# Optimization experiments

Measured on AMD Instinct MI355X. Metric: run time of the kernel, lower is better.

Reference implementation:

```python
import jax, jax.numpy as jnp
import numpy as np
import math

HIDDEN = 1024
N_HEADS = 16
HEAD_DIM = HIDDEN // N_HEADS
N_BLOCKS = 16
BATCH = 2
SEQ = 4096


def setup_inputs() -> dict:
    key = jax.random.key(0)
    ks = jax.random.split(key, 8)
    attention_input = jax.random.normal(ks[0], (BATCH, SEQ, HIDDEN), dtype=jnp.float32)
    attention_mask = jnp.ones((BATCH, SEQ), dtype=jnp.float32)
    # permutation over the num_blocks*num_heads flattened (block, head) axis
    permutation = jax.random.permutation(ks[1], N_BLOCKS * N_HEADS)
    init = 0.02
    q_w = jax.random.normal(ks[2], (HIDDEN, N_HEADS, HEAD_DIM), dtype=jnp.float32) * init
    q_b = jax.random.normal(ks[3], (N_HEADS, HEAD_DIM), dtype=jnp.float32) * init
    k_w = jax.random.normal(ks[4], (HIDDEN, N_HEADS, HEAD_DIM), dtype=jnp.float32) * init
    k_b = jax.random.normal(ks[5], (N_HEADS, HEAD_DIM), dtype=jnp.float32) * init
    v_w = jax.random.normal(ks[6], (HIDDEN, N_HEADS, HEAD_DIM), dtype=jnp.float32) * init
    v_b = jax.random.normal(ks[7], (N_HEADS, HEAD_DIM), dtype=jnp.float32) * init
    return {"attention_input": attention_input, "attention_mask": attention_mask,
            "permutation": permutation, "q_w": q_w, "q_b": q_b,
            "k_w": k_w, "k_b": k_b, "v_w": v_w, "v_b": v_b}


def reference(attention_input, attention_mask, permutation, q_w, q_b, k_w, k_b, v_w, v_b):
    B = attention_mask.shape[0]
    S = attention_mask.shape[1]
    nb = N_BLOCKS
    nh, d = q_b.shape
    blk = S // nb
    # QKV projections: [B,S,H] x [H,N,D] -> [B,S,N,D]
    q = jnp.einsum('bsh,hnd->bsnd', attention_input, q_w) + q_b
    k = jnp.einsum('bsh,hnd->bsnd', attention_input, k_w) + k_b
    v = jnp.einsum('bsh,hnd->bsnd', attention_input, v_w) + v_b

    def blockify(x):  # [B,S,N,D] -> [B, nb, nh, blk, d]
        return x.reshape(B, nb, blk, nh, d).transpose(0, 1, 3, 2, 4)

    q = blockify(q)
    # flatten (block, head) axis and gather per permutation
    k = blockify(k).reshape(B, nb * nh, blk, d)[:, permutation].reshape(B, nb, nh, blk, d)
    v = blockify(v).reshape(B, nb * nh, blk, d)[:, permutation].reshape(B, nb, nh, blk, d)

    scale = 1.0 / math.sqrt(float(d))
    logits = jnp.einsum('bgnqd,bgnkd->bgnqk', q, k) * scale  # block-local scores
    attn = jax.nn.softmax(logits, axis=-1)  # dropout prob 0 / eval mode
    ctx = jnp.einsum('bgnqk,bgnkd->bgnqd', attn, v)
    # [B,nb,nh,blk,d] -> [B,nb,blk,nh,d] -> [B,S,nh,d]
    return ctx.transpose(0, 1, 3, 2, 4).reshape(B, S, nh, d)
```

## Files before the change

kernel.cpp:

```cpp
#include <hip/hip_runtime.h>
#include <hip/hip_bf16.h>
#include <stdint.h>

typedef __attribute__((ext_vector_type(4))) float f32x4;
typedef __attribute__((ext_vector_type(8))) short s16x8;

__device__ inline short f2bf(float f) {
  union { float f; uint32_t u; } v; v.f = f;
  uint32_t r = v.u + 0x7fffu + ((v.u >> 16) & 1u);
  return (short)(r >> 16);
}

__device__ inline void gload_lds16(const void* g, void* l) {
  __builtin_amdgcn_global_load_lds((const __attribute__((address_space(1))) void*)g,
                                   (__attribute__((address_space(3))) void*)l,
                                   16, 0, 0);
}

__global__ __launch_bounds__(256) void k_convert_x(const float* __restrict__ x,
                                                   short* __restrict__ xb) {
  int i = (blockIdx.x * 256 + threadIdx.x) * 8;
  const float4* p = (const float4*)(x + i);
  float4 a = p[0], b = p[1];
  s16x8 o;
  o[0] = f2bf(a.x); o[1] = f2bf(a.y); o[2] = f2bf(a.z); o[3] = f2bf(a.w);
  o[4] = f2bf(b.x); o[5] = f2bf(b.y); o[6] = f2bf(b.z); o[7] = f2bf(b.w);
  *(s16x8*)(xb + i) = o;
}

__global__ __launch_bounds__(256) void k_transpose_w(const float* __restrict__ qw,
                                                     const float* __restrict__ kw,
                                                     const float* __restrict__ vw,
                                                     short* __restrict__ wt) {
  __shared__ float tile[64][65];
  int a  = blockIdx.x >> 8;
  int t2 = blockIdx.x & 255;
  int k0 = (t2 >> 4) << 6;
  int n0 = (t2 & 15) << 6;
  const float* w = (a == 0) ? qw : (a == 1) ? kw : vw;
  int c = threadIdx.x & 63, rr = threadIdx.x >> 6;
#pragma unroll
  for (int i = 0; i < 16; ++i) {
    int r = i * 4 + rr;
    tile[r][c] = w[(k0 + r) * 1024 + n0 + c];
  }
  __syncthreads();
  short* o = wt + a * 1048576;
#pragma unroll
  for (int i = 0; i < 16; ++i) {
    int r = i * 4 + rr;
    o[(n0 + r) * 1024 + k0 + c] = f2bf(tile[c][r]);
  }
}

__global__ __launch_bounds__(256, 2) void k_gemm(const short* __restrict__ xb,
                                                 const short* __restrict__ wt,
                                                 const float* __restrict__ qbias,
                                                 const float* __restrict__ kbias,
                                                 const float* __restrict__ vbias,
                                                 short* __restrict__ Qo,
                                                 short* __restrict__ Ko,
                                                 short* __restrict__ Vo) {
  __shared__ short lds[36864];
  const int tid = threadIdx.x, lane = tid & 63, wv = tid >> 6;
  const int wm = wv >> 1, wn = wv & 1;
  const int mt = blockIdx.x, by = blockIdx.y;
  const int a = by >> 3;
  const short* asrc = xb + (size_t)(mt * 256) * 1024;
  const short* bsrc = wt + (size_t)a * 1048576 + (size_t)((by & 7) * 128) * 1024;

  int srcA[4], dstA[4], srcB[2], dstB[2];
#pragma unroll
  for (int i = 0; i < 4; ++i) {
    int L = i * 256 + tid, s = L & 31;
    int row = (L >> 5) * 8 + (s >> 2);
    int c = (s & 3) ^ ((s >> 3) & 3);
    srcA[i] = row * 1024 + c * 8;
    dstA[i] = L * 16;
  }
#pragma unroll
  for (int i = 0; i < 2; ++i) {
    int L = i * 256 + tid, s = L & 31;
    int row = (L >> 5) * 8 + (s >> 2);
    int c = (s & 3) ^ ((s >> 3) & 3);
    srcB[i] = row * 1024 + c * 8;
    dstB[i] = 16384 + L * 16;
  }

  int aoff[8], boff[4];
#pragma unroll
  for (int m = 0; m < 8; ++m) {
    int row = wm * 128 + m * 16 + (lane & 15);
    aoff[m] = ((row >> 3) * 32 + (row & 7) * 4 + ((lane >> 4) ^ ((row >> 1) & 3))) * 16;
  }
#pragma unroll
  for (int n = 0; n < 4; ++n) {
    int row = wn * 64 + n * 16 + (lane & 15);
    boff[n] = 16384 + ((row >> 3) * 32 + (row & 7) * 4 + ((lane >> 4) ^ ((row >> 1) & 3))) * 16;
  }

  f32x4 acc[8][4] = {};

  auto STAGE = [&](int t, int bb) {
    const short* at = asrc + t * 32;
    const short* bt = bsrc + t * 32;
    char* l = (char*)lds + bb;
#pragma unroll
    for (int i = 0; i < 4; ++i) gload_lds16(at + srcA[i], l + dstA[i]);
#pragma unroll
    for (int i = 0; i < 2; ++i) gload_lds16(bt + srcB[i], l + dstB[i]);
  };

  STAGE(0, 0);
  STAGE(1, 24576);
  int bcur = 0, bpre = 49152;

  for (int t = 0; t < 31; ++t) {
    asm volatile("s_waitcnt vmcnt(6)" ::: "memory");
    __builtin_amdgcn_s_barrier();
    asm volatile("" ::: "memory");
    if (t < 30) STAGE(t + 2, bpre);
    const char* bufc = (const char*)lds + bcur;
    s16x8 af[8], bf[4];
#pragma unroll
    for (int m = 0; m < 8; ++m) af[m] = *(const s16x8*)(bufc + aoff[m]);
#pragma unroll
    for (int n = 0; n < 4; ++n) bf[n] = *(const s16x8*)(bufc + boff[n]);
    __builtin_amdgcn_s_setprio(1);
#pragma unroll
    for (int m = 0; m < 8; ++m)
#pragma unroll
      for (int n = 0; n < 4; ++n)
        acc[m][n] = __builtin_amdgcn_mfma_f32_16x16x32_bf16(af[m], bf[n], acc[m][n], 0, 0, 0);
    __builtin_amdgcn_s_setprio(0);
    bcur += 24576; if (bcur == 73728) bcur = 0;
    bpre += 24576; if (bpre == 73728) bpre = 0;
  }
  asm volatile("s_waitcnt vmcnt(0)" ::: "memory");
  __builtin_amdgcn_s_barrier();
  asm volatile("" ::: "memory");
  {
    const char* bufc = (const char*)lds + bcur;
    s16x8 af[8], bf[4];
#pragma unroll
    for (int m = 0; m < 8; ++m) af[m] = *(const s16x8*)(bufc + aoff[m]);
#pragma unroll
    for (int n = 0; n < 4; ++n) bf[n] = *(const s16x8*)(bufc + boff[n]);
    __builtin_amdgcn_s_setprio(1);
#pragma unroll
    for (int m = 0; m < 8; ++m)
#pragma unroll
      for (int n = 0; n < 4; ++n)
        acc[m][n] = __builtin_amdgcn_mfma_f32_16x16x32_bf16(af[m], bf[n], acc[m][n], 0, 0, 0);
    __builtin_amdgcn_s_setprio(0);
  }

  const float* bias = (a == 0) ? qbias : (a == 1) ? kbias : vbias;
  short* outp = (a == 0) ? Qo : (a == 1) ? Ko : Vo;
  int nbase = (by & 7) * 128 + wn * 64;
  int mbase = mt * 256 + wm * 128;
#pragma unroll
  for (int n = 0; n < 4; ++n) {
    int nloc = nbase + n * 16 + (lane & 15);
    float bv = bias[nloc];
#pragma unroll
    for (int m = 0; m < 8; ++m)
#pragma unroll
      for (int r = 0; r < 4; ++r) {
        int mm = mbase + m * 16 + ((lane >> 4) << 2) + r;
        outp[(size_t)mm * 1024 + nloc] = f2bf(acc[m][n][r] + bv);
      }
  }
}

__global__ __launch_bounds__(512) void k_attn(const short* __restrict__ Qb,
                                              const short* __restrict__ Kb,
                                              const short* __restrict__ Vb,
                                              const int* __restrict__ perm,
                                              float* __restrict__ out) {
  __shared__ short Qs[256 * 64];
  __shared__ short Ks[256 * 64];
  __shared__ short Vs[64 * 256];
  __shared__ short Ps[8 * 1024];

  int tid = threadIdx.x;
  int lane = tid & 63, wv = tid >> 6;
  int bx = blockIdx.x;
  int b = bx >> 8, g = (bx >> 4) & 15, n = bx & 15;
  int p = perm[g * 16 + n];
  int pg = p >> 4, ph = p & 15;

  const short* qsrc = Qb + (size_t)(b * 4096 + g * 256) * 1024 + n * 64;
  const short* ksrc = Kb + (size_t)(b * 4096 + pg * 256) * 1024 + ph * 64;
  const short* vsrc = Vb + (size_t)(b * 4096 + pg * 256) * 1024 + ph * 64;

  s16x8 vreg[4];
#pragma unroll
  for (int i = 0; i < 4; ++i) {
    int c = i * 512 + tid;
    int t = c >> 3;
    int d0 = (c & 7) << 3;
    vreg[i] = *(const s16x8*)(vsrc + t * 1024 + d0);
  }
#pragma unroll
  for (int i = 0; i < 4; ++i) {
    int c = i * 512 + tid;
    int row = c >> 3;
    int colb = (c & 7) << 4;
    int sc = colb ^ ((row & 7) << 4);
    gload_lds16(qsrc + row * 1024 + (sc >> 1), (char*)Qs + c * 16);
    gload_lds16(ksrc + row * 1024 + (sc >> 1), (char*)Ks + c * 16);
  }
#pragma unroll
  for (int i = 0; i < 4; ++i) {
    int c = i * 512 + tid;
    int t = c >> 3;
    int d0 = (c & 7) << 3;
#pragma unroll
    for (int j = 0; j < 8; ++j) {
      int d = d0 + j;
      int sl = (d & 7) ^ ((d >> 3) & 7);
      int by = d * 512 + ((t * 2) ^ (sl << 4));
      *(short*)((char*)Vs + by) = vreg[i][j];
    }
  }
  __syncthreads();

  int qr0 = wv * 32;
  f32x4 accS[2][16] = {};
#pragma unroll
  for (int ks = 0; ks < 2; ++ks) {
    int cb = (ks << 6) + ((lane >> 4) << 4);
    s16x8 aq[2];
#pragma unroll
    for (int rf = 0; rf < 2; ++rf) {
      int row = qr0 + rf * 16 + (lane & 15);
      aq[rf] = *(const s16x8*)((const char*)Qs + row * 128 + (cb ^ ((row & 7) << 4)));
    }
#pragma unroll
    for (int cf = 0; cf < 16; ++cf) {
      int row = cf * 16 + (lane & 15);
      s16x8 bk = *(const s16x8*)((const char*)Ks + row * 128 + (cb ^ ((row & 7) << 4)));
      accS[0][cf] = __builtin_amdgcn_mfma_f32_16x16x32_bf16(aq[0], bk, accS[0][cf], 0, 0, 0);
      accS[1][cf] = __builtin_amdgcn_mfma_f32_16x16x32_bf16(aq[1], bk, accS[1][cf], 0, 0, 0);
    }
  }

  const float sc_log2e = 0.125f * 1.44269504088896f;
  float mx[2][4], inv[2][4];
#pragma unroll
  for (int rf = 0; rf < 2; ++rf)
#pragma unroll
    for (int r = 0; r < 4; ++r) {
      float m_ = accS[rf][0][r];
#pragma unroll
      for (int cf = 1; cf < 16; ++cf) m_ = fmaxf(m_, accS[rf][cf][r]);
#pragma unroll
      for (int msk = 1; msk < 16; msk <<= 1) m_ = fmaxf(m_, __shfl_xor(m_, msk));
      mx[rf][r] = m_;
    }
#pragma unroll
  for (int rf = 0; rf < 2; ++rf)
#pragma unroll
    for (int r = 0; r < 4; ++r) {
      float s_ = 0.f;
#pragma unroll
      for (int cf = 0; cf < 16; ++cf) {
        float e = exp2f((accS[rf][cf][r] - mx[rf][r]) * sc_log2e);
        accS[rf][cf][r] = e;
        s_ += e;
      }
#pragma unroll
      for (int msk = 1; msk < 16; msk <<= 1) s_ += __shfl_xor(s_, msk);
      inv[rf][r] = 1.0f / s_;
    }

  f32x4 accO[2][4] = {};
  short* pchunk = Ps + wv * 1024;
#pragma unroll
  for (int ks = 0; ks < 8; ++ks) {
#pragma unroll
    for (int rf = 0; rf < 2; ++rf)
#pragma unroll
      for (int half = 0; half < 2; ++half) {
        int cf = ks * 2 + half;
        int kvl = half * 16 + (lane & 15);
        int qp = (lane >> 4) << 2;
        int base = rf * 512 + ((kvl >> 3) << 7) + (kvl & 7);
#pragma unroll
        for (int r = 0; r < 4; ++r)
          pchunk[base + (qp + r) * 8] = f2bf(accS[rf][cf][r]);
      }
    int cbv = (ks << 6) + ((lane >> 4) << 4);
#pragma unroll
    for (int rf = 0; rf < 2; ++rf) {
      s16x8 ap = *(const s16x8*)(pchunk + rf * 512 + lane * 8);
#pragma unroll
      for (int dc = 0; dc < 4; ++dc) {
        int vrow = dc * 16 + (lane & 15);
        int sl = (vrow & 7) ^ ((vrow >> 3) & 7);
        s16x8 bv = *(const s16x8*)((const char*)Vs + vrow * 512 + (cbv ^ (sl << 4)));
        accO[rf][dc] = __builtin_amdgcn_mfma_f32_16x16x32_bf16(ap, bv, accO[rf][dc], 0, 0, 0);
      }
    }
  }

#pragma unroll
  for (int rf = 0; rf < 2; ++rf)
#pragma unroll
    for (int dc = 0; dc < 4; ++dc)
#pragma unroll
      for (int r = 0; r < 4; ++r) {
        int q = qr0 + rf * 16 + ((lane >> 4) << 2) + r;
        int d = dc * 16 + (lane & 15);
        out[(size_t)((b * 4096 + g * 256 + q) * 16 + n) * 64 + d] = accO[rf][dc][r] * inv[rf][r];
      }
}

extern "C" void kernel_launch(void* const* d_in, const int* in_sizes, int n_in,
                              void* d_out, int out_size, void* d_ws, size_t ws_size,
                              hipStream_t stream) {
  const float* x    = (const float*)d_in[0];
  const int*   perm = (const int*)d_in[2];
  const float* qw   = (const float*)d_in[3];
  const float* qb   = (const float*)d_in[4];
  const float* kw   = (const float*)d_in[5];
  const float* kb   = (const float*)d_in[6];
  const float* vw   = (const float*)d_in[7];
  const float* vb   = (const float*)d_in[8];
  float* out = (float*)d_out;

  char* ws = (char*)d_ws;
  short* Xb = (short*)(ws);
  short* Wt = (short*)(ws + 16777216UL);
  short* Qb = (short*)(ws + 23068672UL);
  short* Kb = (short*)(ws + 39845888UL);
  short* Vb = (short*)(ws + 56623104UL);

  k_convert_x<<<4096, 256, 0, stream>>>(x, Xb);
  k_transpose_w<<<768, 256, 0, stream>>>(qw, kw, vw, Wt);
  k_gemm<<<dim3(32, 24), 256, 0, stream>>>(Xb, Wt, qb, kb, vb, Qb, Kb, Vb);
  k_attn<<<512, 512, 0, stream>>>(Qb, Kb, Vb, perm, out);
}
```

Before: 106.0 us.

## Fuse QKV GEMM into single 256x192 tile kernel with interleaved output

The projection GEMM is restructured to treat Q, K and V weights as one 1024x3072 matrix. It uses 512-thread workgroups with 256x192 tiles, a K-step of 64, a triple-buffered A and double-buffered B LDS pipeline, and a remapped workgroup order for L2 locality. Output is written as one interleaved [tokens, 3072] buffer that the attention kernel reads with the new stride, and biases are concatenated with device-to-device copies. The aim is to raise MFMA density and data reuse per workgroup and to get a 512-tile grid that fills the CUs better. The cost is three extra memcpy launches and much more LDS per block, which may limit occupancy.

```diff
diff --git a/kernel.cpp b/kernel.cpp
--- a/kernel.cpp
+++ b/kernel.cpp
@@ -16,6 +16,8 @@
                                    (__attribute__((address_space(3))) void*)l,
                                    16, 0, 0);
 }
+
+#define MFMA16 __builtin_amdgcn_mfma_f32_16x16x32_bf16
 
 __global__ __launch_bounds__(256) void k_convert_x(const float* __restrict__ x,
                                                    short* __restrict__ xb) {
@@ -53,129 +55,134 @@
   }
 }
 
-__global__ __launch_bounds__(256, 2) void k_gemm(const short* __restrict__ xb,
+__global__ __launch_bounds__(512, 2) void k_gemm(const short* __restrict__ xb,
                                                  const short* __restrict__ wt,
-                                                 const float* __restrict__ qbias,
-                                                 const float* __restrict__ kbias,
-                                                 const float* __restrict__ vbias,
-                                                 short* __restrict__ Qo,
-                                                 short* __restrict__ Ko,
-                                                 short* __restrict__ Vo) {
-  __shared__ short lds[36864];
+                                                 const float* __restrict__ bias3,
+                                                 short* __restrict__ C) {
+  __shared__ short lds[73728];
   const int tid = threadIdx.x, lane = tid & 63, wv = tid >> 6;
-  const int wm = wv >> 1, wn = wv & 1;
-  const int mt = blockIdx.x, by = blockIdx.y;
-  const int a = by >> 3;
+  const int wm = wv >> 2, wn = wv & 3;
+  int wg = blockIdx.x;
+  wg = (wg & 7) * 64 + (wg >> 3);
+  const int mt = wg >> 4, nt = wg & 15;
   const short* asrc = xb + (size_t)(mt * 256) * 1024;
-  const short* bsrc = wt + (size_t)a * 1048576 + (size_t)((by & 7) * 128) * 1024;
-
-  int srcA[4], dstA[4], srcB[2], dstB[2];
+  const short* bsrc = wt + (size_t)(nt * 192) * 1024;
+
+  int srcA[4], srcB[3];
 #pragma unroll
   for (int i = 0; i < 4; ++i) {
-    int L = i * 256 + tid, s = L & 31;
-    int row = (L >> 5) * 8 + (s >> 2);
-    int c = (s & 3) ^ ((s >> 3) & 3);
-    srcA[i] = row * 1024 + c * 8;
-    dstA[i] = L * 16;
-  }
-#pragma unroll
-  for (int i = 0; i < 2; ++i) {
-    int L = i * 256 + tid, s = L & 31;
-    int row = (L >> 5) * 8 + (s >> 2);
-    int c = (s & 3) ^ ((s >> 3) & 3);
-    srcB[i] = row * 1024 + c * 8;
-    dstB[i] = 16384 + L * 16;
-  }
-
-  int aoff[8], boff[4];
+    int c = i * 512 + tid, r = c >> 3, ss = c & 7;
+    srcA[i] = r * 1024 + (ss ^ (r & 7)) * 8;
+  }
+#pragma unroll
+  for (int i = 0; i < 3; ++i) {
+    int c = i * 512 + tid, r = c >> 3, ss = c & 7;
+    srcB[i] = r * 1024 + (ss ^ (r & 7)) * 8;
+  }
+  int aoff[8], boff[3];
 #pragma unroll
   for (int m = 0; m < 8; ++m) {
-    int row = wm * 128 + m * 16 + (lane & 15);
-    aoff[m] = ((row >> 3) * 32 + (row & 7) * 4 + ((lane >> 4) ^ ((row >> 1) & 3))) * 16;
-  }
-#pragma unroll
-  for (int n = 0; n < 4; ++n) {
-    int row = wn * 64 + n * 16 + (lane & 15);
-    boff[n] = 16384 + ((row >> 3) * 32 + (row & 7) * 4 + ((lane >> 4) ^ ((row >> 1) & 3))) * 16;
-  }
-
-  f32x4 acc[8][4] = {};
-
-  auto STAGE = [&](int t, int bb) {
-    const short* at = asrc + t * 32;
-    const short* bt = bsrc + t * 32;
-    char* l = (char*)lds + bb;
-#pragma unroll
-    for (int i = 0; i < 4; ++i) gload_lds16(at + srcA[i], l + dstA[i]);
-#pragma unroll
-    for (int i = 0; i < 2; ++i) gload_lds16(bt + srcB[i], l + dstB[i]);
+    int r = wm * 128 + m * 16 + (lane & 15);
+    aoff[m] = r * 128 + (((lane >> 4) ^ (r & 7)) << 4);
+  }
+#pragma unroll
+  for (int n = 0; n < 3; ++n) {
+    int r = wn * 48 + n * 16 + (lane & 15);
+    boff[n] = r * 128 + (((lane >> 4) ^ (r & 7)) << 4);
+  }
+
+  f32x4 acc[8][3] = {};
+
+  auto STAGE_A = [&](int t, int slot) {
+    const short* at = asrc + t * 64;
+    char* l = (char*)lds + slot * 32768;
+#pragma unroll
+    for (int i = 0; i < 4; ++i) gload_lds16(at + srcA[i], l + (i * 512 + tid) * 16);
   };
-
-  STAGE(0, 0);
-  STAGE(1, 24576);
-  int bcur = 0, bpre = 49152;
-
-  for (int t = 0; t < 31; ++t) {
-    asm volatile("s_waitcnt vmcnt(6)" ::: "memory");
+  auto STAGE_B = [&](int t, int slot) {
+    const short* bt = bsrc + t * 64;
+    char* l = (char*)lds + 98304 + slot * 24576;
+#pragma unroll
+    for (int i = 0; i < 3; ++i) gload_lds16(bt + srcB[i], l + (i * 512 + tid) * 16);
+  };
+
+  auto COMPUTE = [&](int i) {
+    const char* ab = (const char*)lds + (i % 3) * 32768;
+    const char* bb = (const char*)lds + 98304 + (i & 1) * 24576;
+    s16x8 bfr[3][2], afr[4][2];
+#pragma unroll
+    for (int n = 0; n < 3; ++n) {
+      bfr[n][0] = *(const s16x8*)(bb + boff[n]);
+      bfr[n][1] = *(const s16x8*)(bb + (boff[n] ^ 64));
+    }
+#pragma unroll
+    for (int m = 0; m < 4; ++m) {
+      afr[m][0] = *(const s16x8*)(ab + aoff[m]);
+      afr[m][1] = *(const s16x8*)(ab + (aoff[m] ^ 64));
+    }
+    asm volatile("s_waitcnt lgkmcnt(0)" ::: "memory");
+    __builtin_amdgcn_sched_barrier(0);
+    __builtin_amdgcn_s_setprio(1);
+#pragma unroll
+    for (int m = 0; m < 4; ++m)
+#pragma unroll
+      for (int n = 0; n < 3; ++n) {
+        acc[m][n] = MFMA16(afr[m][0], bfr[n][0], acc[m][n], 0, 0, 0);
+        acc[m][n] = MFMA16(afr[m][1], bfr[n][1], acc[m][n], 0, 0, 0);
+      }
+    __builtin_amdgcn_s_setprio(0);
+#pragma unroll
+    for (int m = 0; m < 4; ++m) {
+      afr[m][0] = *(const s16x8*)(ab + aoff[m + 4]);
+      afr[m][1] = *(const s16x8*)(ab + (aoff[m + 4] ^ 64));
+    }
+    asm volatile("s_waitcnt lgkmcnt(0)" ::: "memory");
+    __builtin_amdgcn_sched_barrier(0);
+    __builtin_amdgcn_s_setprio(1);
+#pragma unroll
+    for (int m = 0; m < 4; ++m)
+#pragma unroll
+      for (int n = 0; n < 3; ++n) {
+        acc[m + 4][n] = MFMA16(afr[m][0], bfr[n][0], acc[m + 4][n], 0, 0, 0);
+        acc[m + 4][n] = MFMA16(afr[m][1], bfr[n][1], acc[m + 4][n], 0, 0, 0);
+      }
+    __builtin_amdgcn_s_setprio(0);
+  };
+
+  STAGE_B(0, 0);
+  STAGE_A(0, 0);
+  STAGE_A(1, 1);
+
+  for (int i = 0; i < 15; ++i) {
+    asm volatile("s_waitcnt vmcnt(4)" ::: "memory");
     __builtin_amdgcn_s_barrier();
     asm volatile("" ::: "memory");
-    if (t < 30) STAGE(t + 2, bpre);
-    const char* bufc = (const char*)lds + bcur;
-    s16x8 af[8], bf[4];
-#pragma unroll
-    for (int m = 0; m < 8; ++m) af[m] = *(const s16x8*)(bufc + aoff[m]);
-#pragma unroll
-    for (int n = 0; n < 4; ++n) bf[n] = *(const s16x8*)(bufc + boff[n]);
-    __builtin_amdgcn_s_setprio(1);
-#pragma unroll
-    for (int m = 0; m < 8; ++m)
-#pragma unroll
-      for (int n = 0; n < 4; ++n)
-        acc[m][n] = __builtin_amdgcn_mfma_f32_16x16x32_bf16(af[m], bf[n], acc[m][n], 0, 0, 0);
-    __builtin_amdgcn_s_setprio(0);
-    bcur += 24576; if (bcur == 73728) bcur = 0;
-    bpre += 24576; if (bpre == 73728) bpre = 0;
+    STAGE_B(i + 1, (i + 1) & 1);
+    if (i < 14) STAGE_A(i + 2, (i + 2) % 3);
+    COMPUTE(i);
   }
   asm volatile("s_waitcnt vmcnt(0)" ::: "memory");
   __builtin_amdgcn_s_barrier();
   asm volatile("" ::: "memory");
-  {
-    const char* bufc = (const char*)lds + bcur;
-    s16x8 af[8], bf[4];
-#pragma unroll
-    for (int m = 0; m < 8; ++m) af[m] = *(const s16x8*)(bufc + aoff[m]);
-#pragma unroll
-    for (int n = 0; n < 4; ++n) bf[n] = *(const s16x8*)(bufc + boff[n]);
-    __builtin_amdgcn_s_setprio(1);
-#pragma unroll
-    for (int m = 0; m < 8; ++m)
-#pragma unroll
-      for (int n = 0; n < 4; ++n)
-        acc[m][n] = __builtin_amdgcn_mfma_f32_16x16x32_bf16(af[m], bf[n], acc[m][n], 0, 0, 0);
-    __builtin_amdgcn_s_setprio(0);
-  }
-
-  const float* bias = (a == 0) ? qbias : (a == 1) ? kbias : vbias;
-  short* outp = (a == 0) ? Qo : (a == 1) ? Ko : Vo;
-  int nbase = (by & 7) * 128 + wn * 64;
+  COMPUTE(15);
+
+  int nbase = nt * 192 + wn * 48;
   int mbase = mt * 256 + wm * 128;
 #pragma unroll
-  for (int n = 0; n < 4; ++n) {
-    int nloc = nbase + n * 16 + (lane & 15);
-    float bv = bias[nloc];
+  for (int n = 0; n < 3; ++n) {
+    int col = nbase + n * 16 + (lane & 15);
+    float bv = bias3[col];
 #pragma unroll
     for (int m = 0; m < 8; ++m)
 #pragma unroll
       for (int r = 0; r < 4; ++r) {
         int mm = mbase + m * 16 + ((lane >> 4) << 2) + r;
-        outp[(size_t)mm * 1024 + nloc] = f2bf(acc[m][n][r] + bv);
-      }
-  }
-}
-
-__global__ __launch_bounds__(512) void k_attn(const short* __restrict__ Qb,
-                                              const short* __restrict__ Kb,
-                                              const short* __restrict__ Vb,
+        C[(size_t)mm * 3072 + col] = f2bf(acc[m][n][r] + bv);
+      }
+  }
+}
+
+__global__ __launch_bounds__(512) void k_attn(const short* __restrict__ QKV,
                                               const int* __restrict__ perm,
                                               float* __restrict__ out) {
   __shared__ short Qs[256 * 64];
@@ -190,9 +197,9 @@
   int p = perm[g * 16 + n];
   int pg = p >> 4, ph = p & 15;
 
-  const short* qsrc = Qb + (size_t)(b * 4096 + g * 256) * 1024 + n * 64;
-  const short* ksrc = Kb + (size_t)(b * 4096 + pg * 256) * 1024 + ph * 64;
-  const short* vsrc = Vb + (size_t)(b * 4096 + pg * 256) * 1024 + ph * 64;
+  const short* qsrc = QKV + (size_t)(b * 4096 + g * 256) * 3072 + n * 64;
+  const short* ksrc = QKV + (size_t)(b * 4096 + pg * 256) * 3072 + 1024 + ph * 64;
+  const short* vsrc = QKV + (size_t)(b * 4096 + pg * 256) * 3072 + 2048 + ph * 64;
 
   s16x8 vreg[4];
 #pragma unroll
@@ -200,7 +207,7 @@
     int c = i * 512 + tid;
     int t = c >> 3;
     int d0 = (c & 7) << 3;
-    vreg[i] = *(const s16x8*)(vsrc + t * 1024 + d0);
+    vreg[i] = *(const s16x8*)(vsrc + t * 3072 + d0);
   }
 #pragma unroll
   for (int i = 0; i < 4; ++i) {
@@ -208,8 +215,8 @@
     int row = c >> 3;
     int colb = (c & 7) << 4;
     int sc = colb ^ ((row & 7) << 4);
-    gload_lds16(qsrc + row * 1024 + (sc >> 1), (char*)Qs + c * 16);
-    gload_lds16(ksrc + row * 1024 + (sc >> 1), (char*)Ks + c * 16);
+    gload_lds16(qsrc + row * 3072 + (sc >> 1), (char*)Qs + c * 16);
+    gload_lds16(ksrc + row * 3072 + (sc >> 1), (char*)Ks + c * 16);
   }
 #pragma unroll
   for (int i = 0; i < 4; ++i) {
@@ -241,8 +248,8 @@
     for (int cf = 0; cf < 16; ++cf) {
       int row = cf * 16 + (lane & 15);
       s16x8 bk = *(const s16x8*)((const char*)Ks + row * 128 + (cb ^ ((row & 7) << 4)));
-      accS[0][cf] = __builtin_amdgcn_mfma_f32_16x16x32_bf16(aq[0], bk, accS[0][cf], 0, 0, 0);
-      accS[1][cf] = __builtin_amdgcn_mfma_f32_16x16x32_bf16(aq[1], bk, accS[1][cf], 0, 0, 0);
+      accS[0][cf] = MFMA16(aq[0], bk, accS[0][cf], 0, 0, 0);
+      accS[1][cf] = MFMA16(aq[1], bk, accS[1][cf], 0, 0, 0);
     }
   }
 
@@ -300,7 +307,7 @@
         int vrow = dc * 16 + (lane & 15);
         int sl = (vrow & 7) ^ ((vrow >> 3) & 7);
         s16x8 bv = *(const s16x8*)((const char*)Vs + vrow * 512 + (cbv ^ (sl << 4)));
-        accO[rf][dc] = __builtin_amdgcn_mfma_f32_16x16x32_bf16(ap, bv, accO[rf][dc], 0, 0, 0);
+        accO[rf][dc] = MFMA16(ap, bv, accO[rf][dc], 0, 0, 0);
       }
     }
   }
@@ -331,14 +338,17 @@
   float* out = (float*)d_out;
 
   char* ws = (char*)d_ws;
-  short* Xb = (short*)(ws);
-  short* Wt = (short*)(ws + 16777216UL);
-  short* Qb = (short*)(ws + 23068672UL);
-  short* Kb = (short*)(ws + 39845888UL);
-  short* Vb = (short*)(ws + 56623104UL);
+  short* Xb    = (short*)(ws);
+  short* Wt    = (short*)(ws + 16777216UL);
+  short* C     = (short*)(ws + 23068672UL);
+  float* bias3 = (float*)(ws + 73400320UL);
+
+  hipMemcpyAsync(bias3,        qb, 4096, hipMemcpyDeviceToDevice, stream);
+  hipMemcpyAsync(bias3 + 1024, kb, 4096, hipMemcpyDeviceToDevice, stream);
+  hipMemcpyAsync(bias3 + 2048, vb, 4096, hipMemcpyDeviceToDevice, stream);
 
   k_convert_x<<<4096, 256, 0, stream>>>(x, Xb);
   k_transpose_w<<<768, 256, 0, stream>>>(qw, kw, vw, Wt);
-  k_gemm<<<dim3(32, 24), 256, 0, stream>>>(Xb, Wt, qb, kb, vb, Qb, Kb, Vb);
-  k_attn<<<512, 512, 0, stream>>>(Qb, Kb, Vb, perm, out);
-}
+  k_gemm<<<512, 512, 0, stream>>>(Xb, Wt, bias3, C);
+  k_attn<<<512, 512, 0, stream>>>(C, perm, out);
+}
```

Result: slower. 118.6 us (+11.9%).

## Split attention blocks into query halves with shared Q/P LDS buffer

Applied to the files above, without the earlier changes.

The attention kernel now launches 1024 workgroups of 256 threads, each handling half the query rows (128) of a block-head pair instead of all 256 with 512 threads. The Q tile and the P staging buffer share one LDS region, separated by an added barrier, so LDS per block drops and two blocks can fit per CU. Workgroup indices are remapped so consecutive blocks are spread across XCDs. The trade-off is that each K/V tile is now loaded twice, once per query half, doubling K/V reads and the V transpose work.

```diff
diff --git a/kernel.cpp b/kernel.cpp
--- a/kernel.cpp
+++ b/kernel.cpp
@@ -16,6 +16,8 @@
                                    (__attribute__((address_space(3))) void*)l,
                                    16, 0, 0);
 }
+
+#define MFMA16 __builtin_amdgcn_mfma_f32_16x16x32_bf16
 
 __global__ __launch_bounds__(256) void k_convert_x(const float* __restrict__ x,
                                                    short* __restrict__ xb) {
@@ -131,7 +133,7 @@
     for (int m = 0; m < 8; ++m)
 #pragma unroll
       for (int n = 0; n < 4; ++n)
-        acc[m][n] = __builtin_amdgcn_mfma_f32_16x16x32_bf16(af[m], bf[n], acc[m][n], 0, 0, 0);
+        acc[m][n] = MFMA16(af[m], bf[n], acc[m][n], 0, 0, 0);
     __builtin_amdgcn_s_setprio(0);
     bcur += 24576; if (bcur == 73728) bcur = 0;
     bpre += 24576; if (bpre == 73728) bpre = 0;
@@ -151,7 +153,7 @@
     for (int m = 0; m < 8; ++m)
 #pragma unroll
       for (int n = 0; n < 4; ++n)
-        acc[m][n] = __builtin_amdgcn_mfma_f32_16x16x32_bf16(af[m], bf[n], acc[m][n], 0, 0, 0);
+        acc[m][n] = MFMA16(af[m], bf[n], acc[m][n], 0, 0, 0);
     __builtin_amdgcn_s_setprio(0);
   }
 
@@ -173,47 +175,52 @@
   }
 }
 
-__global__ __launch_bounds__(512) void k_attn(const short* __restrict__ Qb,
-                                              const short* __restrict__ Kb,
-                                              const short* __restrict__ Vb,
-                                              const int* __restrict__ perm,
-                                              float* __restrict__ out) {
-  __shared__ short Qs[256 * 64];
+__global__ __launch_bounds__(256, 2) void k_attn(const short* __restrict__ Qb,
+                                                 const short* __restrict__ Kb,
+                                                 const short* __restrict__ Vb,
+                                                 const int* __restrict__ perm,
+                                                 float* __restrict__ out) {
   __shared__ short Ks[256 * 64];
   __shared__ short Vs[64 * 256];
-  __shared__ short Ps[8 * 1024];
+  __shared__ short QP[8192];
 
   int tid = threadIdx.x;
   int lane = tid & 63, wv = tid >> 6;
   int bx = blockIdx.x;
-  int b = bx >> 8, g = (bx >> 4) & 15, n = bx & 15;
+  int wg = (bx & 7) * 128 + (bx >> 3);
+  int b = wg >> 9, g = (wg >> 5) & 15, n = (wg >> 1) & 15, h = wg & 1;
   int p = perm[g * 16 + n];
   int pg = p >> 4, ph = p & 15;
 
-  const short* qsrc = Qb + (size_t)(b * 4096 + g * 256) * 1024 + n * 64;
+  const short* qsrc = Qb + (size_t)(b * 4096 + g * 256 + h * 128) * 1024 + n * 64;
   const short* ksrc = Kb + (size_t)(b * 4096 + pg * 256) * 1024 + ph * 64;
   const short* vsrc = Vb + (size_t)(b * 4096 + pg * 256) * 1024 + ph * 64;
 
-  s16x8 vreg[4];
-#pragma unroll
-  for (int i = 0; i < 4; ++i) {
-    int c = i * 512 + tid;
+  s16x8 vreg[8];
+#pragma unroll
+  for (int i = 0; i < 8; ++i) {
+    int c = i * 256 + tid;
     int t = c >> 3;
     int d0 = (c & 7) << 3;
     vreg[i] = *(const s16x8*)(vsrc + t * 1024 + d0);
   }
 #pragma unroll
   for (int i = 0; i < 4; ++i) {
-    int c = i * 512 + tid;
+    int c = i * 256 + tid;
     int row = c >> 3;
-    int colb = (c & 7) << 4;
-    int sc = colb ^ ((row & 7) << 4);
-    gload_lds16(qsrc + row * 1024 + (sc >> 1), (char*)Qs + c * 16);
+    int sc = ((c & 7) << 4) ^ ((row & 7) << 4);
+    gload_lds16(qsrc + row * 1024 + (sc >> 1), (char*)QP + c * 16);
+  }
+#pragma unroll
+  for (int i = 0; i < 8; ++i) {
+    int c = i * 256 + tid;
+    int row = c >> 3;
+    int sc = ((c & 7) << 4) ^ ((row & 7) << 4);
     gload_lds16(ksrc + row * 1024 + (sc >> 1), (char*)Ks + c * 16);
   }
 #pragma unroll
-  for (int i = 0; i < 4; ++i) {
-    int c = i * 512 + tid;
+  for (int i = 0; i < 8; ++i) {
+    int c = i * 256 + tid;
     int t = c >> 3;
     int d0 = (c & 7) << 3;
 #pragma unroll
@@ -235,14 +242,14 @@
 #pragma unroll
     for (int rf = 0; rf < 2; ++rf) {
       int row = qr0 + rf * 16 + (lane & 15);
-      aq[rf] = *(const s16x8*)((const char*)Qs + row * 128 + (cb ^ ((row & 7) << 4)));
+      aq[rf] = *(const s16x8*)((const char*)QP + row * 128 + (cb ^ ((row & 7) << 4)));
     }
 #pragma unroll
     for (int cf = 0; cf < 16; ++cf) {
       int row = cf * 16 + (lane & 15);
       s16x8 bk = *(const s16x8*)((const char*)Ks + row * 128 + (cb ^ ((row & 7) << 4)));
-      accS[0][cf] = __builtin_amdgcn_mfma_f32_16x16x32_bf16(aq[0], bk, accS[0][cf], 0, 0, 0);
-      accS[1][cf] = __builtin_amdgcn_mfma_f32_16x16x32_bf16(aq[1], bk, accS[1][cf], 0, 0, 0);
+      accS[0][cf] = MFMA16(aq[0], bk, accS[0][cf], 0, 0, 0);
+      accS[1][cf] = MFMA16(aq[1], bk, accS[1][cf], 0, 0, 0);
     }
   }
 
@@ -275,8 +282,10 @@
       inv[rf][r] = 1.0f / s_;
     }
 
+  __syncthreads();
+
   f32x4 accO[2][4] = {};
-  short* pchunk = Ps + wv * 1024;
+  short* pchunk = QP + wv * 1024;
 #pragma unroll
   for (int ks = 0; ks < 8; ++ks) {
 #pragma unroll
@@ -300,7 +309,7 @@
         int vrow = dc * 16 + (lane & 15);
         int sl = (vrow & 7) ^ ((vrow >> 3) & 7);
         s16x8 bv = *(const s16x8*)((const char*)Vs + vrow * 512 + (cbv ^ (sl << 4)));
-        accO[rf][dc] = __builtin_amdgcn_mfma_f32_16x16x32_bf16(ap, bv, accO[rf][dc], 0, 0, 0);
+        accO[rf][dc] = MFMA16(ap, bv, accO[rf][dc], 0, 0, 0);
       }
     }
   }
@@ -311,7 +320,7 @@
     for (int dc = 0; dc < 4; ++dc)
 #pragma unroll
       for (int r = 0; r < 4; ++r) {
-        int q = qr0 + rf * 16 + ((lane >> 4) << 2) + r;
+        int q = h * 128 + qr0 + rf * 16 + ((lane >> 4) << 2) + r;
         int d = dc * 16 + (lane & 15);
         out[(size_t)((b * 4096 + g * 256 + q) * 16 + n) * 64 + d] = accO[rf][dc][r] * inv[rf][r];
       }
@@ -340,5 +349,5 @@
   k_convert_x<<<4096, 256, 0, stream>>>(x, Xb);
   k_transpose_w<<<768, 256, 0, stream>>>(qw, kw, vw, Wt);
   k_gemm<<<dim3(32, 24), 256, 0, stream>>>(Xb, Wt, qb, kb, vb, Qb, Kb, Vb);
-  k_attn<<<512, 512, 0, stream>>>(Qb, Kb, Vb, perm, out);
-}
+  k_attn<<<1024, 256, 0, stream>>>(Qb, Kb, Vb, perm, out);
+}
```

Result: faster. 101.3 us (-4.5%).
